# Optimization experiments

Measured on AMD Instinct MI355X. Metric: run time of the kernel, lower is better.

Reference implementation:

```python
import jax, jax.numpy as jnp
import numpy as np

B, V, J, K, G, L, E = 8, 262144, 64, 4, 2048, 8, 1835008


def _qmul(q1, q2):
    # quaternion product, (w, x, y, z) convention; broadcasts over leading dims
    w1, v1 = q1[..., :1], q1[..., 1:]
    w2, v2 = q2[..., :1], q2[..., 1:]
    w = w1 * w2 - jnp.sum(v1 * v2, axis=-1, keepdims=True)
    v = w1 * v2 + w2 * v1 + jnp.cross(v1, v2)
    return jnp.concatenate([w, v], axis=-1)


def _qrot(q, v):
    # rotate vector v by unit quaternion q (w, x, y, z)
    qv, qw = q[..., 1:], q[..., :1]
    return v + 2.0 * jnp.cross(qv, jnp.cross(qv, v) + qw * v)


def setup_inputs() -> dict:
    key = jax.random.key(0)
    ks = jax.random.split(key, 13)
    return {
        "temp_verts": jax.random.normal(ks[0], (V, 3), dtype=jnp.float32),
        "joint_quat": jax.random.normal(ks[1], (B, J, 4), dtype=jnp.float32),
        "joint_trans": jax.random.normal(ks[2], (B, J, 3), dtype=jnp.float32),
        "skin_w": jax.random.uniform(ks[3], (V, K), dtype=jnp.float32),
        "node_pos": jax.random.normal(ks[4], (G, 3), dtype=jnp.float32),
        "node_quat": jax.random.normal(ks[5], (B, G, 4), dtype=jnp.float32),
        "node_trans": jax.random.normal(ks[6], (B, G, 3), dtype=jnp.float32),
        "link_w": jax.random.uniform(ks[7], (V, L), dtype=jnp.float32),
        "lap_w": jax.random.normal(ks[8], (E,), dtype=jnp.float32) * 0.1,
        "skin_idx": jax.random.randint(ks[9], (V, K), 0, J),
        "link_idx": jax.random.randint(ks[10], (V, L), 0, G),
        "lap_st": jax.random.randint(ks[11], (E,), 0, V),
        "lap_ed": jax.random.randint(ks[12], (E,), 0, V),
    }


def reference(temp_verts, joint_quat, joint_trans, skin_w, node_pos, node_quat,
              node_trans, link_w, lap_w, skin_idx, link_idx, lap_st, lap_ed):
    eps = 1e-8
    # ----- embedded-graph deformation of the template -----
    lw = link_w / (jnp.sum(link_w, axis=-1, keepdims=True) + eps)      # [V,L]
    nq = node_quat[:, link_idx]                                        # [B,V,L,4]
    nq = nq / (jnp.linalg.norm(nq, axis=-1, keepdims=True) + eps)
    nt = node_trans[:, link_idx]                                       # [B,V,L,3]
    gp = node_pos[link_idx]                                            # [V,L,3]
    local = temp_verts[:, None, :] - gp                                # [V,L,3]
    warped = _qrot(nq, local[None]) + gp[None] + nt                    # [B,V,L,3]
    v_eg = jnp.sum(lw[None, :, :, None] * warped, axis=2)              # [B,V,3]

    # ----- dual-quaternion skinning -----
    jq = joint_quat / (jnp.linalg.norm(joint_quat, axis=-1, keepdims=True) + eps)  # [B,J,4]
    t0 = jnp.concatenate([jnp.zeros_like(joint_trans[..., :1]), joint_trans], axis=-1)
    jd = 0.5 * _qmul(t0, jq)                                           # dual part [B,J,4]

    sw = skin_w / (jnp.sum(skin_w, axis=-1, keepdims=True) + eps)      # [V,K]
    r = jq[:, skin_idx]                                                # [B,V,K,4]
    d = jd[:, skin_idx]                                                # [B,V,K,4]
    # sign-fix against first influence to avoid antipodal blending
    sgn = jnp.where(jnp.sum(r * r[..., :1, :], axis=-1, keepdims=True) >= 0.0, 1.0, -1.0)
    w = sw[None, :, :, None] * sgn                                     # [B,V,K,1]
    rb = jnp.sum(w * r, axis=2)                                        # [B,V,4]
    db = jnp.sum(w * d, axis=2)                                        # [B,V,4]
    nrm = jnp.linalg.norm(rb, axis=-1, keepdims=True) + eps
    rb, db = rb / nrm, db / nrm
    rw, rv = rb[..., :1], rb[..., 1:]
    dw, dv = db[..., :1], db[..., 1:]
    trans = 2.0 * (rw * dv - dw * rv + jnp.cross(rv, dv))              # [B,V,3]
    posed = _qrot(rb, v_eg) + trans                                    # [B,V,3]

    # ----- sparse Laplacian regularization term (COO scatter) -----
    def _lap(p):
        return jax.ops.segment_sum(lap_w[:, None] * p[lap_ed], lap_st, num_segments=V)
    lap = jax.vmap(_lap)(posed)                                        # [B,V,3]

    return jnp.stack([posed, lap], axis=0)                             # [2,B,V,3]
```

## Files before the change

kernel.cpp:

```cpp
#include <hip/hip_runtime.h>
#include <hip/hip_bf16.h>
#include <math.h>

constexpr int B = 8;
constexpr int V = 262144;
constexpr int J = 64;
constexpr int K = 4;
constexpr int G = 2048;
constexpr int L = 8;
constexpr int E = 1835008;
constexpr float EPS = 1e-8f;
constexpr int PT6 = 512;
constexpr int NB2 = 256;
constexpr int VB2 = V / NB2;
constexpr int PBLK = 256;
constexpr int EPP = E / PBLK;
constexpr int CHK = 4096;

__device__ inline unsigned bf16bits(float x) {
  unsigned u = __float_as_uint(x);
  return (u + 0x7fffu + ((u >> 16) & 1u)) >> 16;
}
__device__ inline float bflo(unsigned u) { return __uint_as_float(u << 16); }
__device__ inline float bfhi(unsigned u) {
  return __uint_as_float(u & 0xffff0000u);
}

__global__ __launch_bounds__(256) void jqd_kernel(
    const float* __restrict__ jquat, const float* __restrict__ jtrans,
    float* __restrict__ ws) {
  int i = blockIdx.x * blockDim.x + threadIdx.x;
  if (i >= B * J) return;
  float qw = jquat[i * 4 + 0];
  float qx = jquat[i * 4 + 1];
  float qy = jquat[i * 4 + 2];
  float qz = jquat[i * 4 + 3];
  float inv = 1.0f / (sqrtf(qw * qw + qx * qx + qy * qy + qz * qz) + EPS);
  qw *= inv; qx *= inv; qy *= inv; qz *= inv;
  float tx = jtrans[i * 3 + 0];
  float ty = jtrans[i * 3 + 1];
  float tz = jtrans[i * 3 + 2];
  float dw = -0.5f * (tx * qx + ty * qy + tz * qz);
  float dx = 0.5f * (qw * tx + (ty * qz - tz * qy));
  float dy = 0.5f * (qw * ty + (tz * qx - tx * qz));
  float dz = 0.5f * (qw * tz + (tx * qy - ty * qx));
  float* o = ws + (size_t)i * 8;
  o[0] = qw; o[1] = qx; o[2] = qy; o[3] = qz;
  o[4] = dw; o[5] = dx; o[6] = dy; o[7] = dz;
}

__global__ __launch_bounds__(256) void nmat16_kernel(
    const float* __restrict__ npos, const float* __restrict__ nquat,
    const float* __restrict__ ntrans, unsigned* __restrict__ nmt16) {
  int i = blockIdx.x * blockDim.x + threadIdx.x;
  if (i >= B * G) return;
  int g = i & (G - 1);
  float4 q = *reinterpret_cast<const float4*>(nquat + (size_t)i * 4);
  float qw = q.x, qx = q.y, qy = q.z, qz = q.w;
  float inv = 1.0f / (sqrtf(qw * qw + qx * qx + qy * qy + qz * qz) + EPS);
  qw *= inv; qx *= inv; qy *= inv; qz *= inv;
  float xx = qx * qx, yy = qy * qy, zz = qz * qz;
  float xy = qx * qy, xz = qx * qz, yz = qy * qz;
  float wx = qw * qx, wy = qw * qy, wz = qw * qz;
  float m00 = 1.f - 2.f * (yy + zz), m01 = 2.f * (xy - wz), m02 = 2.f * (xz + wy);
  float m10 = 2.f * (xy + wz), m11 = 1.f - 2.f * (xx + zz), m12 = 2.f * (yz - wx);
  float m20 = 2.f * (xz - wy), m21 = 2.f * (yz + wx), m22 = 1.f - 2.f * (xx + yy);
  float gx = npos[g * 3 + 0], gy = npos[g * 3 + 1], gz = npos[g * 3 + 2];
  float tx = ntrans[(size_t)i * 3 + 0] + gx - (m00 * gx + m01 * gy + m02 * gz);
  float ty = ntrans[(size_t)i * 3 + 1] + gy - (m10 * gx + m11 * gy + m12 * gz);
  float tz = ntrans[(size_t)i * 3 + 2] + gz - (m20 * gx + m21 * gy + m22 * gz);
  unsigned* o = nmt16 + (size_t)i * 6;
  o[0] = bf16bits(m00) | (bf16bits(m01) << 16);
  o[1] = bf16bits(m02) | (bf16bits(tx) << 16);
  o[2] = bf16bits(m10) | (bf16bits(m11) << 16);
  o[3] = bf16bits(m12) | (bf16bits(ty) << 16);
  o[4] = bf16bits(m20) | (bf16bits(m21) << 16);
  o[5] = bf16bits(m22) | (bf16bits(tz) << 16);
}

__global__ __launch_bounds__(PT6, 4) void posed6_kernel(
    const float* __restrict__ tv, const float* __restrict__ sw_in,
    const float* __restrict__ lw_in, const int* __restrict__ sidx,
    const int* __restrict__ lidx, const unsigned* __restrict__ nmt16,
    const float* __restrict__ jqd, float* __restrict__ out,
    unsigned* __restrict__ pvm16, int mode) {
  __shared__ unsigned smu[G * 6];
  int v = blockIdx.x * PT6 + threadIdx.x;

  float px = tv[(size_t)v * 3 + 0];
  float py = tv[(size_t)v * 3 + 1];
  float pz = tv[(size_t)v * 3 + 2];

  int4 si = *reinterpret_cast<const int4*>(sidx + (size_t)v * 4);
  float4 swv = *reinterpret_cast<const float4*>(sw_in + (size_t)v * 4);
  int4 li0 = *reinterpret_cast<const int4*>(lidx + (size_t)v * 8);
  int4 li1 = *reinterpret_cast<const int4*>(lidx + (size_t)v * 8 + 4);
  float4 lw0 = *reinterpret_cast<const float4*>(lw_in + (size_t)v * 8);
  float4 lw1 = *reinterpret_cast<const float4*>(lw_in + (size_t)v * 8 + 4);

  float sinv = 1.0f / (swv.x + swv.y + swv.z + swv.w + EPS);
  float swn[K] = {swv.x * sinv, swv.y * sinv, swv.z * sinv, swv.w * sinv};
  int sj[K] = {si.x, si.y, si.z, si.w};

  float linv =
      1.0f / (lw0.x + lw0.y + lw0.z + lw0.w + lw1.x + lw1.y + lw1.z + lw1.w + EPS);
  float lwn[L] = {lw0.x * linv, lw0.y * linv, lw0.z * linv, lw0.w * linv,
                  lw1.x * linv, lw1.y * linv, lw1.z * linv, lw1.w * linv};
  int gi[L] = {li0.x * 6, li0.y * 6, li0.z * 6, li0.w * 6,
               li1.x * 6, li1.y * 6, li1.z * 6, li1.w * 6};

  constexpr size_t LAPOFF = (size_t)B * V * 3;
  unsigned pk[2 * B];

  for (int b = 0; b < B; ++b) {
    __syncthreads();
    const uint4* src = reinterpret_cast<const uint4*>(nmt16 + (size_t)b * G * 6);
    uint4* dst = reinterpret_cast<uint4*>(smu);
#pragma unroll
    for (int it = 0; it < (G * 6 / 4) / PT6; ++it) {
      int q = it * PT6 + threadIdx.x;
      dst[q] = src[q];
    }
    __syncthreads();

    float ex = 0.f, ey = 0.f, ez = 0.f;
#pragma unroll
    for (int l = 0; l < L; ++l) {
      const uint2* nb = reinterpret_cast<const uint2*>(smu + gi[l]);
      uint2 u0 = nb[0], u1 = nb[1], u2 = nb[2];
      float w = lwn[l];
      ex += w * (bflo(u0.x) * px + bfhi(u0.x) * py + bflo(u0.y) * pz + bfhi(u0.y));
      ey += w * (bflo(u1.x) * px + bfhi(u1.x) * py + bflo(u1.y) * pz + bfhi(u1.y));
      ez += w * (bflo(u2.x) * px + bfhi(u2.x) * py + bflo(u2.y) * pz + bfhi(u2.y));
    }

    float rbw = 0.f, rbx = 0.f, rby = 0.f, rbz = 0.f;
    float dbw = 0.f, dbx = 0.f, dby = 0.f, dbz = 0.f;
    float r0w = 0.f, r0x = 0.f, r0y = 0.f, r0z = 0.f;
#pragma unroll
    for (int k = 0; k < K; ++k) {
      const float* eptr = jqd + ((size_t)b * J + sj[k]) * 8;
      float4 qf = *reinterpret_cast<const float4*>(eptr);
      float4 df = *reinterpret_cast<const float4*>(eptr + 4);
      float qw = qf.x, qx = qf.y, qy = qf.z, qz = qf.w;
      if (k == 0) { r0w = qw; r0x = qx; r0y = qy; r0z = qz; }
      float dotr = qw * r0w + qx * r0x + qy * r0y + qz * r0z;
      float s = (dotr >= 0.0f) ? swn[k] : -swn[k];
      rbw += s * qw; rbx += s * qx; rby += s * qy; rbz += s * qz;
      dbw += s * df.x; dbx += s * df.y; dby += s * df.z; dbz += s * df.w;
    }
    float ninv = 1.0f / (sqrtf(rbw * rbw + rbx * rbx + rby * rby + rbz * rbz) + EPS);
    rbw *= ninv; rbx *= ninv; rby *= ninv; rbz *= ninv;
    dbw *= ninv; dbx *= ninv; dby *= ninv; dbz *= ninv;

    float txx = 2.0f * (rbw * dbx - dbw * rbx + (rby * dbz - rbz * dby));
    float tyy = 2.0f * (rbw * dby - dbw * rby + (rbz * dbx - rbx * dbz));
    float tzz = 2.0f * (rbw * dbz - dbw * rbz + (rbx * dby - rby * dbx));

    float cx = rby * ez - rbz * ey + rbw * ex;
    float cy = rbz * ex - rbx * ez + rbw * ey;
    float cz = rbx * ey - rby * ex + rbw * ez;
    float ox = ex + 2.0f * (rby * cz - rbz * cy) + txx;
    float oy = ey + 2.0f * (rbz * cx - rbx * cz) + tyy;
    float oz = ez + 2.0f * (rbx * cy - rby * cx) + tzz;

    size_t o = ((size_t)b * V + v) * 3;
    out[o + 0] = ox; out[o + 1] = oy; out[o + 2] = oz;
    pk[b * 2 + 0] = bf16bits(ox) | (bf16bits(oy) << 16);
    pk[b * 2 + 1] = bf16bits(oz);
    if (mode == 2) {
      out[LAPOFF + o + 0] = 0.f;
      out[LAPOFF + o + 1] = 0.f;
      out[LAPOFF + o + 2] = 0.f;
    }
  }

  if (mode == 0) {
    uint4* dst = reinterpret_cast<uint4*>(pvm16 + (size_t)v * 16);
    dst[0] = make_uint4(pk[0], pk[1], pk[2], pk[3]);
    dst[1] = make_uint4(pk[4], pk[5], pk[6], pk[7]);
    dst[2] = make_uint4(pk[8], pk[9], pk[10], pk[11]);
    dst[3] = make_uint4(pk[12], pk[13], pk[14], pk[15]);
  }
}

__global__ __launch_bounds__(256) void cnt256_kernel(const int* __restrict__ st,
                                                     int* __restrict__ bcnt) {
  __shared__ int h[NB2];
  int blk = blockIdx.x, t = threadIdx.x;
  h[t] = 0;
  __syncthreads();
  int e0 = blk * EPP;
  for (int i = e0 + t; i < e0 + EPP; i += 256) atomicAdd(&h[st[i] >> 10], 1);
  __syncthreads();
  bcnt[t * PBLK + blk] = h[t];
}

__global__ __launch_bounds__(256) void scanA_kernel(const int* __restrict__ in,
                                                    int* __restrict__ out,
                                                    int* __restrict__ bs) {
  __shared__ int s[256];
  int t = threadIdx.x;
  int i = blockIdx.x * 256 + t;
  int x = in[i];
  s[t] = x;
  __syncthreads();
  for (int off = 1; off < 256; off <<= 1) {
    int v = (t >= off) ? s[t - off] : 0;
    __syncthreads();
    s[t] += v;
    __syncthreads();
  }
  out[i] = s[t] - x;
  if (t == 255) bs[blockIdx.x] = s[t];
}

__global__ __launch_bounds__(256) void scanB_kernel(int* __restrict__ bs) {
  __shared__ int s[256];
  int t = threadIdx.x;
  int x = bs[t];
  s[t] = x;
  __syncthreads();
  for (int off = 1; off < 256; off <<= 1) {
    int v = (t >= off) ? s[t - off] : 0;
    __syncthreads();
    s[t] += v;
    __syncthreads();
  }
  bs[t] = s[t] - x;
}

__global__ __launch_bounds__(256) void scanC_kernel(int* __restrict__ out,
                                                    const int* __restrict__ bs) {
  out[blockIdx.x * 256 + threadIdx.x] += bs[blockIdx.x];
}

__global__ __launch_bounds__(256) void part256_kernel(
    const int* __restrict__ st, const int* __restrict__ ed,
    const float* __restrict__ w, const int* __restrict__ boff2,
    int2* __restrict__ ewB) {
  __shared__ int lbase[NB2];
  __shared__ int lcur[NB2];
  int blk = blockIdx.x, t = threadIdx.x;
  lbase[t] = boff2[t * PBLK + blk];
  lcur[t] = 0;
  __syncthreads();
  int e0 = blk * EPP;
  for (int i = e0 + t; i < e0 + EPP; i += 256) {
    int s = st[i];
    int b = s >> 10;
    int pos = lbase[b] + atomicAdd(&lcur[b], 1);
    ewB[pos] = make_int2(((s & 1023) << 18) | ed[i], __float_as_int(w[i]));
  }
}

__global__ __launch_bounds__(1024) void lap_sorted_kernel(
    const int2* __restrict__ ewB, const int* __restrict__ boff2,
    const unsigned* __restrict__ pvm16, float* __restrict__ lap) {
  __shared__ int2 eL[CHK];
  __shared__ int rs[VB2];
  __shared__ int cur[VB2];
  int p = blockIdx.x, t = threadIdx.x;
  int beg = boff2[p * PBLK];
  int end = (p < NB2 - 1) ? boff2[(p + 1) * PBLK] : E;

  float acc[24];
#pragma unroll
  for (int i = 0; i < 24; ++i) acc[i] = 0.f;

  for (int cbeg = beg; cbeg < end; cbeg += CHK) {
    int cnt = min(CHK, end - cbeg);
    rs[t] = 0;
    __syncthreads();

    int2 er[CHK / 1024];
#pragma unroll
    for (int j = 0; j < CHK / 1024; ++j) {
      int idx = j * 1024 + t;
      if (idx < cnt) {
        er[j] = ewB[cbeg + idx];
        atomicAdd(&rs[((unsigned)er[j].x) >> 18], 1);
      }
    }
    __syncthreads();

    int x = rs[t];
    for (int off = 1; off < VB2; off <<= 1) {
      int v = (t >= off) ? rs[t - off] : 0;
      __syncthreads();
      rs[t] += v;
      __syncthreads();
    }
    int excl = rs[t] - x;
    __syncthreads();
    rs[t] = excl;
    cur[t] = excl;
    __syncthreads();

#pragma unroll
    for (int j = 0; j < CHK / 1024; ++j) {
      int idx = j * 1024 + t;
      if (idx < cnt) {
        int sl = ((unsigned)er[j].x) >> 18;
        int pos = atomicAdd(&cur[sl], 1);
        eL[pos] = er[j];
      }
    }
    __syncthreads();

    int rbeg = rs[t];
    int rend = (t < VB2 - 1) ? rs[t + 1] : cnt;
    for (int j = rbeg; j < rend; ++j) {
      int2 ew = eL[j];
      float w = __int_as_float(ew.y);
      int d = ew.x & 0x3ffff;
      const uint4* q = reinterpret_cast<const uint4*>(pvm16 + (size_t)d * 16);
      uint4 q0 = q[0], q1 = q[1], q2 = q[2], q3 = q[3];
      unsigned u[16] = {q0.x, q0.y, q0.z, q0.w, q1.x, q1.y, q1.z, q1.w,
                        q2.x, q2.y, q2.z, q2.w, q3.x, q3.y, q3.z, q3.w};
#pragma unroll
      for (int b = 0; b < B; ++b) {
        acc[b * 3 + 0] += w * bflo(u[2 * b]);
        acc[b * 3 + 1] += w * bfhi(u[2 * b]);
        acc[b * 3 + 2] += w * bflo(u[2 * b + 1]);
      }
    }
    __syncthreads();
  }

  int v = p * VB2 + t;
#pragma unroll
  for (int b = 0; b < B; ++b) {
    size_t o = ((size_t)b * V + v) * 3;
    lap[o + 0] = acc[b * 3 + 0];
    lap[o + 1] = acc[b * 3 + 1];
    lap[o + 2] = acc[b * 3 + 2];
  }
}

__global__ __launch_bounds__(256) void lap_atomic_kernel(
    const float* __restrict__ lapw, const int* __restrict__ st,
    const int* __restrict__ ed, const float* __restrict__ posed,
    float* __restrict__ lap) {
  int e = blockIdx.x * blockDim.x + threadIdx.x;
  if (e >= E) return;
  float w = lapw[e];
  int s = st[e];
  int d = ed[e];
#pragma unroll
  for (int b = 0; b < B; ++b) {
    size_t pb = ((size_t)b * V + d) * 3;
    size_t ob = ((size_t)b * V + s) * 3;
    atomicAdd(&lap[ob + 0], w * posed[pb + 0]);
    atomicAdd(&lap[ob + 1], w * posed[pb + 1]);
    atomicAdd(&lap[ob + 2], w * posed[pb + 2]);
  }
}

extern "C" void kernel_launch(void* const* d_in, const int* in_sizes, int n_in,
                              void* d_out, int out_size, void* d_ws, size_t ws_size,
                              hipStream_t stream) {
  const float* tv    = (const float*)d_in[0];
  const float* jquat = (const float*)d_in[1];
  const float* jtran = (const float*)d_in[2];
  const float* sw    = (const float*)d_in[3];
  const float* npos  = (const float*)d_in[4];
  const float* nquat = (const float*)d_in[5];
  const float* ntran = (const float*)d_in[6];
  const float* lw    = (const float*)d_in[7];
  const float* lapw  = (const float*)d_in[8];
  const int*   sidx  = (const int*)d_in[9];
  const int*   lidx  = (const int*)d_in[10];
  const int*   lst   = (const int*)d_in[11];
  const int*   led   = (const int*)d_in[12];
  float* out = (float*)d_out;
  float* lap = out + (size_t)B * V * 3;

  float*    jqd   = (float*)d_ws;
  unsigned* nmt16 = (unsigned*)(jqd + 4096);
  int*      bcnt  = (int*)(nmt16 + (size_t)B * G * 6);
  int*      boff2 = bcnt + NB2 * PBLK;
  int*      bsum  = boff2 + NB2 * PBLK;
  int2*     ewB   = (int2*)(bsum + 256 + 60);
  unsigned* pvm16 = (unsigned*)(ewB + E);
  size_t need = (size_t)((char*)(pvm16 + (size_t)V * 16) - (char*)d_ws);
  int tier = (ws_size >= need) ? 0 : 2;

  jqd_kernel<<<(B * J + 255) / 256, 256, 0, stream>>>(jquat, jtran, jqd);
  nmat16_kernel<<<(B * G + 255) / 256, 256, 0, stream>>>(npos, nquat, ntran,
                                                         nmt16);

  if (tier == 0) {
    cnt256_kernel<<<PBLK, 256, 0, stream>>>(lst, bcnt);
    scanA_kernel<<<NB2, 256, 0, stream>>>(bcnt, boff2, bsum);
    scanB_kernel<<<1, 256, 0, stream>>>(bsum);
    scanC_kernel<<<NB2, 256, 0, stream>>>(boff2, bsum);
    part256_kernel<<<PBLK, 256, 0, stream>>>(lst, led, lapw, boff2, ewB);
    posed6_kernel<<<V / PT6, PT6, 0, stream>>>(tv, sw, lw, sidx, lidx, nmt16,
                                               jqd, out, pvm16, 0);
    lap_sorted_kernel<<<NB2, 1024, 0, stream>>>(ewB, boff2, pvm16, lap);
  } else {
    posed6_kernel<<<V / PT6, PT6, 0, stream>>>(tv, sw, lw, sidx, lidx, nmt16,
                                               jqd, out, (unsigned*)jqd, 2);
    lap_atomic_kernel<<<E / 256, 256, 0, stream>>>(lapw, lst, led, out, lap);
  }
}
```

Baseline: 180.4 us.

## Split posed kernel batch loop across two blocks with 1024-thread blocks

```diff
diff --git a/kernel.cpp b/kernel.cpp
--- a/kernel.cpp
+++ b/kernel.cpp
@@ -10,7 +10,9 @@
 constexpr int L = 8;
 constexpr int E = 1835008;
 constexpr float EPS = 1e-8f;
-constexpr int PT6 = 512;
+constexpr int PT7 = 1024;
+constexpr int BH = 2;
+constexpr int NBH = B / BH;
 constexpr int NB2 = 256;
 constexpr int VB2 = V / NB2;
 constexpr int PBLK = 256;
@@ -78,14 +80,16 @@
   o[5] = bf16bits(m22) | (bf16bits(tz) << 16);
 }
 
-__global__ __launch_bounds__(PT6, 4) void posed6_kernel(
+__global__ __launch_bounds__(PT7) void posed7_kernel(
     const float* __restrict__ tv, const float* __restrict__ sw_in,
     const float* __restrict__ lw_in, const int* __restrict__ sidx,
     const int* __restrict__ lidx, const unsigned* __restrict__ nmt16,
     const float* __restrict__ jqd, float* __restrict__ out,
     unsigned* __restrict__ pvm16, int mode) {
   __shared__ unsigned smu[G * 6];
-  int v = blockIdx.x * PT6 + threadIdx.x;
+  int bh = blockIdx.x & (BH - 1);
+  int v = (blockIdx.x >> 1) * PT7 + threadIdx.x;
+  int b0 = bh * NBH;
 
   float px = tv[(size_t)v * 3 + 0];
   float py = tv[(size_t)v * 3 + 1];
@@ -110,15 +114,16 @@
                li1.x * 6, li1.y * 6, li1.z * 6, li1.w * 6};
 
   constexpr size_t LAPOFF = (size_t)B * V * 3;
-  unsigned pk[2 * B];
-
-  for (int b = 0; b < B; ++b) {
+  unsigned pk[2 * NBH];
+
+  for (int bi = 0; bi < NBH; ++bi) {
+    int b = b0 + bi;
     __syncthreads();
     const uint4* src = reinterpret_cast<const uint4*>(nmt16 + (size_t)b * G * 6);
     uint4* dst = reinterpret_cast<uint4*>(smu);
 #pragma unroll
-    for (int it = 0; it < (G * 6 / 4) / PT6; ++it) {
-      int q = it * PT6 + threadIdx.x;
+    for (int it = 0; it < (G * 6 / 4) / PT7; ++it) {
+      int q = it * PT7 + threadIdx.x;
       dst[q] = src[q];
     }
     __syncthreads();
@@ -166,8 +171,8 @@
 
     size_t o = ((size_t)b * V + v) * 3;
     out[o + 0] = ox; out[o + 1] = oy; out[o + 2] = oz;
-    pk[b * 2 + 0] = bf16bits(ox) | (bf16bits(oy) << 16);
-    pk[b * 2 + 1] = bf16bits(oz);
+    pk[bi * 2 + 0] = bf16bits(ox) | (bf16bits(oy) << 16);
+    pk[bi * 2 + 1] = bf16bits(oz);
     if (mode == 2) {
       out[LAPOFF + o + 0] = 0.f;
       out[LAPOFF + o + 1] = 0.f;
@@ -176,11 +181,9 @@
   }
 
   if (mode == 0) {
-    uint4* dst = reinterpret_cast<uint4*>(pvm16 + (size_t)v * 16);
+    uint4* dst = reinterpret_cast<uint4*>(pvm16 + (size_t)v * 16 + bh * 8);
     dst[0] = make_uint4(pk[0], pk[1], pk[2], pk[3]);
     dst[1] = make_uint4(pk[4], pk[5], pk[6], pk[7]);
-    dst[2] = make_uint4(pk[8], pk[9], pk[10], pk[11]);
-    dst[3] = make_uint4(pk[12], pk[13], pk[14], pk[15]);
   }
 }
 
@@ -396,12 +399,12 @@
     scanB_kernel<<<1, 256, 0, stream>>>(bsum);
     scanC_kernel<<<NB2, 256, 0, stream>>>(boff2, bsum);
     part256_kernel<<<PBLK, 256, 0, stream>>>(lst, led, lapw, boff2, ewB);
-    posed6_kernel<<<V / PT6, PT6, 0, stream>>>(tv, sw, lw, sidx, lidx, nmt16,
-                                               jqd, out, pvm16, 0);
+    posed7_kernel<<<(V / PT7) * BH, PT7, 0, stream>>>(
+        tv, sw, lw, sidx, lidx, nmt16, jqd, out, pvm16, 0);
     lap_sorted_kernel<<<NB2, 1024, 0, stream>>>(ewB, boff2, pvm16, lap);
   } else {
-    posed6_kernel<<<V / PT6, PT6, 0, stream>>>(tv, sw, lw, sidx, lidx, nmt16,
-                                               jqd, out, (unsigned*)jqd, 2);
+    posed7_kernel<<<(V / PT7) * BH, PT7, 0, stream>>>(
+        tv, sw, lw, sidx, lidx, nmt16, jqd, out, (unsigned*)jqd, 2);
     lap_atomic_kernel<<<E / 256, 256, 0, stream>>>(lapw, lst, led, out, lap);
   }
 }
```

Result: faster. 175.8 us (-2.6%).

## Double-buffer node tables in LDS with register prefetch and SoA layout

Applied to the files above, without the earlier changes.

```diff
diff --git a/kernel.cpp b/kernel.cpp
--- a/kernel.cpp
+++ b/kernel.cpp
@@ -10,12 +10,15 @@
 constexpr int L = 8;
 constexpr int E = 1835008;
 constexpr float EPS = 1e-8f;
-constexpr int PT6 = 512;
+constexpr int PT8 = 1024;
 constexpr int NB2 = 256;
 constexpr int VB2 = V / NB2;
 constexpr int PBLK = 256;
 constexpr int EPP = E / PBLK;
 constexpr int CHK = 4096;
+constexpr int NODE_U2 = G * 3;
+constexpr int JQ_OFF = 4 * NODE_U2;
+constexpr int LDS_U32 = 2 * G * 6 + 2 * 512;
 
 __device__ inline unsigned bf16bits(float x) {
   unsigned u = __float_as_uint(x);
@@ -78,14 +81,16 @@
   o[5] = bf16bits(m22) | (bf16bits(tz) << 16);
 }
 
-__global__ __launch_bounds__(PT6, 4) void posed6_kernel(
+__global__ __launch_bounds__(PT8) void posed8_kernel(
     const float* __restrict__ tv, const float* __restrict__ sw_in,
     const float* __restrict__ lw_in, const int* __restrict__ sidx,
     const int* __restrict__ lidx, const unsigned* __restrict__ nmt16,
-    const float* __restrict__ jqd, float* __restrict__ out,
+    const float* __restrict__ jq, float* __restrict__ out,
     unsigned* __restrict__ pvm16, int mode) {
-  __shared__ unsigned smu[G * 6];
-  int v = blockIdx.x * PT6 + threadIdx.x;
+  extern __shared__ unsigned sm8[];
+  uint2* lds2 = reinterpret_cast<uint2*>(sm8);
+  int t = threadIdx.x;
+  int v = blockIdx.x * PT8 + t;
 
   float px = tv[(size_t)v * 3 + 0];
   float py = tv[(size_t)v * 3 + 1];
@@ -106,40 +111,64 @@
       1.0f / (lw0.x + lw0.y + lw0.z + lw0.w + lw1.x + lw1.y + lw1.z + lw1.w + EPS);
   float lwn[L] = {lw0.x * linv, lw0.y * linv, lw0.z * linv, lw0.w * linv,
                   lw1.x * linv, lw1.y * linv, lw1.z * linv, lw1.w * linv};
-  int gi[L] = {li0.x * 6, li0.y * 6, li0.z * 6, li0.w * 6,
-               li1.x * 6, li1.y * 6, li1.z * 6, li1.w * 6};
+  int gi[L] = {li0.x, li0.y, li0.z, li0.w, li1.x, li1.y, li1.z, li1.w};
 
   constexpr size_t LAPOFF = (size_t)B * V * 3;
   unsigned pk[2 * B];
 
+  uint2 stA[6];
+  uint2 stJ;
+
+  {
+    const uint2* src = reinterpret_cast<const uint2*>(nmt16);
+#pragma unroll
+    for (int k = 0; k < 6; ++k) stA[k] = src[t + k * PT8];
+    if (t < 256) stJ = reinterpret_cast<const uint2*>(jq)[t];
+  }
+
   for (int b = 0; b < B; ++b) {
-    __syncthreads();
-    const uint4* src = reinterpret_cast<const uint4*>(nmt16 + (size_t)b * G * 6);
-    uint4* dst = reinterpret_cast<uint4*>(smu);
-#pragma unroll
-    for (int it = 0; it < (G * 6 / 4) / PT6; ++it) {
-      int q = it * PT6 + threadIdx.x;
-      dst[q] = src[q];
-    }
-    __syncthreads();
-
+    int buf = b & 1;
+    __syncthreads();
+#pragma unroll
+    for (int k = 0; k < 6; ++k) {
+      int id = t + k * PT8;
+      int g = id / 3;
+      int wp = id - 3 * g;
+      lds2[buf * NODE_U2 + wp * G + g] = stA[k];
+    }
+    if (t < 256)
+      reinterpret_cast<uint2*>(sm8 + JQ_OFF + buf * 512)[t] = stJ;
+    if (b < B - 1) {
+      const uint2* src =
+          reinterpret_cast<const uint2*>(nmt16) + (size_t)(b + 1) * (G * 3);
+#pragma unroll
+      for (int k = 0; k < 6; ++k) stA[k] = src[t + k * PT8];
+      if (t < 256)
+        stJ = reinterpret_cast<const uint2*>(jq)[(size_t)(b + 1) * 256 + t];
+    }
+    __syncthreads();
+
+    const uint2* nb = lds2 + buf * NODE_U2;
     float ex = 0.f, ey = 0.f, ez = 0.f;
 #pragma unroll
     for (int l = 0; l < L; ++l) {
-      const uint2* nb = reinterpret_cast<const uint2*>(smu + gi[l]);
-      uint2 u0 = nb[0], u1 = nb[1], u2 = nb[2];
+      int g = gi[l];
+      uint2 u0 = nb[g];
+      uint2 u1 = nb[G + g];
+      uint2 u2 = nb[2 * G + g];
       float w = lwn[l];
       ex += w * (bflo(u0.x) * px + bfhi(u0.x) * py + bflo(u0.y) * pz + bfhi(u0.y));
       ey += w * (bflo(u1.x) * px + bfhi(u1.x) * py + bflo(u1.y) * pz + bfhi(u1.y));
       ez += w * (bflo(u2.x) * px + bfhi(u2.x) * py + bflo(u2.y) * pz + bfhi(u2.y));
     }
 
+    const float* jbase = reinterpret_cast<const float*>(sm8 + JQ_OFF + buf * 512);
     float rbw = 0.f, rbx = 0.f, rby = 0.f, rbz = 0.f;
     float dbw = 0.f, dbx = 0.f, dby = 0.f, dbz = 0.f;
     float r0w = 0.f, r0x = 0.f, r0y = 0.f, r0z = 0.f;
 #pragma unroll
     for (int k = 0; k < K; ++k) {
-      const float* eptr = jqd + ((size_t)b * J + sj[k]) * 8;
+      const float* eptr = jbase + sj[k] * 8;
       float4 qf = *reinterpret_cast<const float4*>(eptr);
       float4 df = *reinterpret_cast<const float4*>(eptr + 4);
       float qw = qf.x, qx = qf.y, qy = qf.z, qz = qf.w;
@@ -396,12 +425,12 @@
     scanB_kernel<<<1, 256, 0, stream>>>(bsum);
     scanC_kernel<<<NB2, 256, 0, stream>>>(boff2, bsum);
     part256_kernel<<<PBLK, 256, 0, stream>>>(lst, led, lapw, boff2, ewB);
-    posed6_kernel<<<V / PT6, PT6, 0, stream>>>(tv, sw, lw, sidx, lidx, nmt16,
-                                               jqd, out, pvm16, 0);
+    posed8_kernel<<<V / PT8, PT8, LDS_U32 * sizeof(unsigned), stream>>>(
+        tv, sw, lw, sidx, lidx, nmt16, jqd, out, pvm16, 0);
     lap_sorted_kernel<<<NB2, 1024, 0, stream>>>(ewB, boff2, pvm16, lap);
   } else {
-    posed6_kernel<<<V / PT6, PT6, 0, stream>>>(tv, sw, lw, sidx, lidx, nmt16,
-                                               jqd, out, (unsigned*)jqd, 2);
+    posed8_kernel<<<V / PT8, PT8, LDS_U32 * sizeof(unsigned), stream>>>(
+        tv, sw, lw, sidx, lidx, nmt16, jqd, out, (unsigned*)jqd, 2);
     lap_atomic_kernel<<<E / 256, 256, 0, stream>>>(lapw, lst, led, out, lap);
   }
 }
```

New measurement: 222.1 us. 1.23x slower.
